# Optimization experiments

Measured on AMD Instinct MI355X. Metric: run time of the kernel, lower is better.

## Reference

```python
import jax, jax.numpy as jnp
import numpy as np

N = 16_777_216  # total samples in batch
S = 1024        # number of distinct stations/basins
EPS = 1e-6


def setup_inputs() -> dict:
    key = jax.random.key(0)
    k1, k2, k3, k4 = jax.random.split(key, 4)
    y_pred = jax.random.normal(k1, (N,), dtype=jnp.float32)
    y_true = jax.random.normal(k2, (N,), dtype=jnp.float32)
    stations = jax.random.randint(k3, (N,), 0, S, dtype=jnp.int32)
    # per-station observed-discharge std (kept away from 0 for realism)
    station_std = jax.random.uniform(k4, (S,), dtype=jnp.float32) + 0.5
    return {"y_pred": y_pred, "y_true": y_true, "stations": stations,
            "station_std": station_std}


def reference(y_pred, y_true, stations, station_std):
    y_pred = y_pred.reshape(-1)
    y_true = y_true.reshape(-1)
    err2 = (y_pred - y_true) ** 2                                   # [N]
    sse = jax.ops.segment_sum(err2, stations, num_segments=S)       # [S]
    cnt = jax.ops.segment_sum(jnp.ones_like(err2), stations, num_segments=S)
    mse = sse / jnp.maximum(cnt, 1.0)                                # per-station MSE
    denom = (station_std + EPS) ** 2                                 # (sigma+eps)^2
    present = cnt > 0                                                # stations in batch
    per_station = jnp.where(present, mse / denom, 0.0)
    n_present = jnp.maximum(jnp.sum(present.astype(jnp.float32)), 1.0)
    return jnp.sum(per_station) / n_present
```

## Files before the change

kernel.cpp:

```cpp
#include <hip/hip_runtime.h>

#define NUM_S 1024
constexpr float EPS = 1e-6f;

constexpr int CNT_SHIFT = 44;
constexpr unsigned long long SSE_MASK = (1ULL << 44) - 1;
constexpr float FP_SCALE = 1048576.0f;
constexpr double FP_INV_SCALE = 1.0 / 1048576.0;

__global__ __launch_bounds__(1024, 2) void nse_partial_kernel(
    const float4* __restrict__ yp4, const float4* __restrict__ yt4,
    const int4* __restrict__ st4, const float* __restrict__ yp,
    const float* __restrict__ yt, const int* __restrict__ st,
    unsigned long long* __restrict__ g_hist, int n, int n4)
{
    __shared__ unsigned long long s_hist[NUM_S];
    for (int i = threadIdx.x; i < NUM_S; i += blockDim.x) {
        s_hist[i] = 0ULL;
    }
    __syncthreads();

    const int gtid = blockIdx.x * blockDim.x + threadIdx.x;
    const int stride = gridDim.x * blockDim.x;
    const unsigned long long ONE_CNT = 1ULL << CNT_SHIFT;

    for (int i = gtid; i < n4; i += stride) {
        float4 p = yp4[i];
        float4 t = yt4[i];
        int4 s = st4[i];
        float dx = p.x - t.x;
        float dy = p.y - t.y;
        float dz = p.z - t.z;
        float dw = p.w - t.w;
        unsigned fx = (unsigned)(dx * dx * FP_SCALE + 0.5f);
        unsigned fy = (unsigned)(dy * dy * FP_SCALE + 0.5f);
        unsigned fz = (unsigned)(dz * dz * FP_SCALE + 0.5f);
        unsigned fw = (unsigned)(dw * dw * FP_SCALE + 0.5f);
        atomicAdd(&s_hist[s.x], ONE_CNT | (unsigned long long)fx);
        atomicAdd(&s_hist[s.y], ONE_CNT | (unsigned long long)fy);
        atomicAdd(&s_hist[s.z], ONE_CNT | (unsigned long long)fz);
        atomicAdd(&s_hist[s.w], ONE_CNT | (unsigned long long)fw);
    }
    for (int i = n4 * 4 + gtid; i < n; i += stride) {
        float d = yp[i] - yt[i];
        unsigned f = (unsigned)(d * d * FP_SCALE + 0.5f);
        atomicAdd(&s_hist[st[i]], ONE_CNT | (unsigned long long)f);
    }
    __syncthreads();

    for (int i = threadIdx.x; i < NUM_S; i += blockDim.x) {
        unsigned long long h = s_hist[i];
        if (h != 0ULL) {
            atomicAdd(&g_hist[i], h);
        }
    }
}

__global__ __launch_bounds__(1024) void nse_final_kernel(
    const unsigned long long* __restrict__ g_hist,
    const float* __restrict__ station_std, float* __restrict__ out)
{
    const int s = threadIdx.x;
    unsigned long long h = g_hist[s];
    float c = (float)(unsigned)(h >> CNT_SHIFT);
    float v = (float)((double)(h & SSE_MASK) * FP_INV_SCALE);
    float sd = station_std[s];
    float denom = (sd + EPS) * (sd + EPS);
    float per = (c > 0.0f) ? (v / fmaxf(c, 1.0f)) / denom : 0.0f;
    float pres = (c > 0.0f) ? 1.0f : 0.0f;

    #pragma unroll
    for (int o = 32; o > 0; o >>= 1) {
        per += __shfl_down(per, o, 64);
        pres += __shfl_down(pres, o, 64);
    }

    __shared__ float w_per[16];
    __shared__ float w_pres[16];
    const int lane = threadIdx.x & 63;
    const int wid = threadIdx.x >> 6;
    if (lane == 0) {
        w_per[wid] = per;
        w_pres[wid] = pres;
    }
    __syncthreads();

    if (wid == 0) {
        float sp = (lane < 16) ? w_per[lane] : 0.0f;
        float sc = (lane < 16) ? w_pres[lane] : 0.0f;
        #pragma unroll
        for (int o = 8; o > 0; o >>= 1) {
            sp += __shfl_down(sp, o, 64);
            sc += __shfl_down(sc, o, 64);
        }
        if (lane == 0) {
            out[0] = sp / fmaxf(sc, 1.0f);
        }
    }
}

extern "C" void kernel_launch(void* const* d_in, const int* in_sizes, int n_in,
                              void* d_out, int out_size, void* d_ws, size_t ws_size,
                              hipStream_t stream) {
    const float* y_pred = (const float*)d_in[0];
    const float* y_true = (const float*)d_in[1];
    const int* stations = (const int*)d_in[2];
    const float* station_std = (const float*)d_in[3];
    float* out = (float*)d_out;

    const int n = in_sizes[0];
    const int n4 = n / 4;

    unsigned long long* g_hist = (unsigned long long*)d_ws;

    hipMemsetAsync(d_ws, 0, NUM_S * sizeof(unsigned long long), stream);

    dim3 grid(512);
    dim3 block(1024);
    nse_partial_kernel<<<grid, block, 0, stream>>>(
        (const float4*)y_pred, (const float4*)y_true, (const int4*)stations,
        y_pred, y_true, stations, g_hist, n, n4);

    nse_final_kernel<<<1, 1024, 0, stream>>>(g_hist, station_std, out);
}
```

Baseline: 199.5 us.

## Replace global histogram atomics with per-block partials and parallel reduce

Each block now writes its shared-memory histogram to its own slice of workspace instead of atomically adding into one global histogram, and the memset is removed by zeroing the control word inside the first kernel. A new 32-block reduce kernel sums the partials per station, computes per-station terms, and finishes with a last-block-done atomic counter. This aims to remove global atomic contention and the memset launch, at the cost of writing and re-reading about 4 MB of partials. Because block 0 resets the counter while other blocks run, the reset's ordering relative to the second kernel relies on the kernel boundary.

```diff
diff --git a/kernel.cpp b/kernel.cpp
--- a/kernel.cpp
+++ b/kernel.cpp
@@ -8,15 +8,24 @@
 constexpr float FP_SCALE = 1048576.0f;
 constexpr double FP_INV_SCALE = 1.0 / 1048576.0;
 
+#define MAX_PBLOCKS 512
+#define RED_BLOCKS 32
+
 __global__ __launch_bounds__(1024, 2) void nse_partial_kernel(
     const float4* __restrict__ yp4, const float4* __restrict__ yt4,
     const int4* __restrict__ st4, const float* __restrict__ yp,
     const float* __restrict__ yt, const int* __restrict__ st,
-    unsigned long long* __restrict__ g_hist, int n, int n4)
+    unsigned long long* __restrict__ g_part,
+    unsigned int* __restrict__ g_ctl, int n, int n4)
 {
     __shared__ unsigned long long s_hist[NUM_S];
     for (int i = threadIdx.x; i < NUM_S; i += blockDim.x) {
         s_hist[i] = 0ULL;
+    }
+    if (blockIdx.x == 0 && threadIdx.x == 0) {
+        g_ctl[0] = 0u;
+        ((float*)g_ctl)[1] = 0.0f;
+        ((float*)g_ctl)[2] = 0.0f;
     }
     __syncthreads();
 
@@ -48,53 +57,67 @@
     }
     __syncthreads();
 
+    unsigned long long* dst = g_part + (size_t)blockIdx.x * NUM_S;
     for (int i = threadIdx.x; i < NUM_S; i += blockDim.x) {
-        unsigned long long h = s_hist[i];
-        if (h != 0ULL) {
-            atomicAdd(&g_hist[i], h);
-        }
+        dst[i] = s_hist[i];
     }
 }
 
-__global__ __launch_bounds__(1024) void nse_final_kernel(
-    const unsigned long long* __restrict__ g_hist,
-    const float* __restrict__ station_std, float* __restrict__ out)
+__global__ __launch_bounds__(1024) void nse_reduce_kernel(
+    const unsigned long long* __restrict__ g_part,
+    const float* __restrict__ station_std,
+    unsigned int* __restrict__ g_ctl,
+    float* __restrict__ out, int nblocks)
 {
-    const int s = threadIdx.x;
-    unsigned long long h = g_hist[s];
-    float c = (float)(unsigned)(h >> CNT_SHIFT);
-    float v = (float)((double)(h & SSE_MASK) * FP_INV_SCALE);
-    float sd = station_std[s];
-    float denom = (sd + EPS) * (sd + EPS);
-    float per = (c > 0.0f) ? (v / fmaxf(c, 1.0f)) / denom : 0.0f;
-    float pres = (c > 0.0f) ? 1.0f : 0.0f;
+    __shared__ unsigned long long s_part[1024];
+    const int t = threadIdx.x;
+    const int s_lo = blockIdx.x * 32;
+    const int ss = s_lo + (t & 31);
+    const int chunk = t >> 5;
+    const int per_chunk = (nblocks + 31) >> 5;
+    const int b0 = chunk * per_chunk;
+    const int b1 = min(b0 + per_chunk, nblocks);
 
-    #pragma unroll
-    for (int o = 32; o > 0; o >>= 1) {
-        per += __shfl_down(per, o, 64);
-        pres += __shfl_down(pres, o, 64);
+    unsigned long long acc = 0ULL;
+    for (int b = b0; b < b1; ++b) {
+        acc += g_part[(size_t)b * NUM_S + ss];
+    }
+    s_part[t] = acc;
+    __syncthreads();
+
+    float per = 0.0f, pres = 0.0f;
+    if (t < 32) {
+        unsigned long long h = 0ULL;
+        #pragma unroll
+        for (int c = 0; c < 32; ++c) {
+            h += s_part[t + (c << 5)];
+        }
+        float cnt = (float)(unsigned)(h >> CNT_SHIFT);
+        if (cnt > 0.0f) {
+            float sse = (float)((double)(h & SSE_MASK) * FP_INV_SCALE);
+            float sd = station_std[s_lo + t];
+            float denom = (sd + EPS) * (sd + EPS);
+            per = (sse / cnt) / denom;
+            pres = 1.0f;
+        }
     }
 
-    __shared__ float w_per[16];
-    __shared__ float w_pres[16];
-    const int lane = threadIdx.x & 63;
-    const int wid = threadIdx.x >> 6;
-    if (lane == 0) {
-        w_per[wid] = per;
-        w_pres[wid] = pres;
-    }
-    __syncthreads();
-
-    if (wid == 0) {
-        float sp = (lane < 16) ? w_per[lane] : 0.0f;
-        float sc = (lane < 16) ? w_pres[lane] : 0.0f;
+    if (t < 64) {
         #pragma unroll
-        for (int o = 8; o > 0; o >>= 1) {
-            sp += __shfl_down(sp, o, 64);
-            sc += __shfl_down(sc, o, 64);
+        for (int o = 32; o > 0; o >>= 1) {
+            per += __shfl_down(per, o, 64);
+            pres += __shfl_down(pres, o, 64);
         }
-        if (lane == 0) {
-            out[0] = sp / fmaxf(sc, 1.0f);
+        if (t == 0) {
+            atomicAdd((float*)g_ctl + 1, per);
+            atomicAdd((float*)g_ctl + 2, pres);
+            __threadfence();
+            unsigned int old = atomicAdd(g_ctl, 1u);
+            if (old == gridDim.x - 1) {
+                float sp = atomicAdd((float*)g_ctl + 1, 0.0f);
+                float sc = atomicAdd((float*)g_ctl + 2, 0.0f);
+                out[0] = sp / fmaxf(sc, 1.0f);
+            }
         }
     }
 }
@@ -111,15 +134,20 @@
     const int n = in_sizes[0];
     const int n4 = n / 4;
 
-    unsigned long long* g_hist = (unsigned long long*)d_ws;
+    unsigned int* g_ctl = (unsigned int*)d_ws;
+    unsigned long long* g_part =
+        (unsigned long long*)((char*)d_ws + 64);
 
-    hipMemsetAsync(d_ws, 0, NUM_S * sizeof(unsigned long long), stream);
+    long long avail = ((long long)ws_size - 64) / (NUM_S * 8);
+    int npart = (int)(avail < 1 ? 1 : (avail > MAX_PBLOCKS ? MAX_PBLOCKS : avail));
 
-    dim3 grid(512);
+    dim3 grid1(npart);
     dim3 block(1024);
-    nse_partial_kernel<<<grid, block, 0, stream>>>(
+    nse_partial_kernel<<<grid1, block, 0, stream>>>(
         (const float4*)y_pred, (const float4*)y_true, (const int4*)stations,
-        y_pred, y_true, stations, g_hist, n, n4);
+        y_pred, y_true, stations, g_part, g_ctl, n, n4);
 
-    nse_final_kernel<<<1, 1024, 0, stream>>>(g_hist, station_std, out);
+    dim3 grid2(RED_BLOCKS);
+    nse_reduce_kernel<<<grid2, block, 0, stream>>>(
+        g_part, station_std, g_ctl, out, npart);
 }
```

New measurement: 203.9 us. 1.02x slower.
